# Kernel optimization log

Hardware: AMD Instinct MI355X
Metric: run time of the kernel (lower is better)

## Reference

```python
import jax, jax.numpy as jnp
import numpy as np

B, W, IN, H, Z, D, OUT, K = 256, 128, 128, 1024, 128, 1024, 128, 3


def _gru_cell(h, x, Wih, Whh, bih, bhh):
    # torch nn.GRU single-layer cell, gate order (r, z, n)
    gi = x @ Wih.T + bih
    gh = h @ Whh.T + bhh
    ir, iz, inn = jnp.split(gi, 3, axis=-1)
    hr, hz, hn = jnp.split(gh, 3, axis=-1)
    r = jax.nn.sigmoid(ir + hr)
    u = jax.nn.sigmoid(iz + hz)
    n = jnp.tanh(inn + r * hn)
    return (1.0 - u) * n + u * h


def setup_inputs():
    key = jax.random.key(0)
    ks = iter(jax.random.split(key, 40))

    def w(shape, fanin):
        return jax.random.normal(next(ks), shape, jnp.float32) / np.float32(np.sqrt(fanin))

    return dict(
        x=jax.random.normal(next(ks), (B, W, IN), jnp.float32),
        eps_q=jax.random.uniform(next(ks), (B, W, Z), jnp.float32),
        eps_p=jax.random.uniform(next(ks), (B, W, OUT), jnp.float32),
        Wih_q=w((3 * H, IN), IN), Whh_q=w((3 * H, H), H),
        bih_q=jnp.zeros(3 * H, jnp.float32), bhh_q=jnp.zeros(3 * H, jnp.float32),
        Wd_q=w((D, Z + H), Z + H), bd_q=jnp.zeros(D, jnp.float32),
        Wmu_q=w((Z, D), D), bmu_q=jnp.zeros(Z, jnp.float32),
        Wsig_q=w((Z, D), D), bsig_q=jnp.zeros(Z, jnp.float32),
        Wp=w((K, Z, Z), Z), bp=jnp.zeros((K, Z), jnp.float32),
        up=0.1 * jax.random.normal(next(ks), (K,), jnp.float32),
        Wlg=w((Z, Z), Z), blg=jnp.zeros(Z, jnp.float32),
        Wih_p=w((3 * H, Z), Z), Whh_p=w((3 * H, H), H),
        bih_p=jnp.zeros(3 * H, jnp.float32), bhh_p=jnp.zeros(3 * H, jnp.float32),
        Wd_p=w((D, H), H), bd_p=jnp.zeros(D, jnp.float32),
        Wmu_p=w((OUT, D), D), bmu_p=jnp.zeros(OUT, jnp.float32),
        Wsig_p=w((OUT, D), D), bsig_p=jnp.zeros(OUT, jnp.float32),
    )


def _forward(x, eps_q, eps_p, Wih_q, Whh_q, bih_q, bhh_q, Wd_q, bd_q, Wmu_q, bmu_q,
             Wsig_q, bsig_q, Wp, bp, up, Wlg, blg, Wih_p, Whh_p, bih_p, bhh_p,
             Wd_p, bd_p, Wmu_p, bmu_p, Wsig_p, bsig_p):
    Bsz = x.shape[0]

    # ---- Qnet: sequential encoder with planar flows ----
    def q_step(carry, inp):
        e, z_prev = carry
        x_t, eps_t = inp  # [B,IN], [B,Z]
        e = _gru_cell(e, x_t, Wih_q, Whh_q, bih_q, bhh_q)
        d = jnp.concatenate([z_prev, e], axis=-1) @ Wd_q.T + bd_q
        mu = d @ Wmu_q.T + bmu_q
        logvar = jax.nn.softplus(d @ Wsig_q.T + bsig_q)
        z = mu + jnp.exp(0.5 * logvar) * eps_t
        for k in range(K):  # planar normalizing flows: z + u * tanh(Wz + b)
            z = z + up[k] * jnp.tanh(z @ Wp[k].T + bp[k])
        return (e, z), (z, mu, logvar)

    e0 = jnp.zeros((Bsz, H), x.dtype)
    z0 = jnp.zeros((Bsz, Z), x.dtype)
    _, (z_seq, mu_seq, lv_seq) = jax.lax.scan(
        q_step, (e0, z0), (jnp.swapaxes(x, 0, 1), jnp.swapaxes(eps_q, 0, 1)))

    # ---- Pnet: sequential decoder ----
    def p_step(d_t, inp):
        z_t, eps_t = inp
        zt = z_t @ Wlg.T + blg  # LGSSM linear
        d_t = _gru_cell(d_t, zt, Wih_p, Whh_p, bih_p, bhh_p)
        dd = d_t @ Wd_p.T + bd_p
        mu = dd @ Wmu_p.T + bmu_p
        sigma = jax.nn.softplus(dd @ Wsig_p.T + bsig_p)
        return d_t, mu + sigma * eps_t

    d0 = jnp.zeros((Bsz, H), x.dtype)
    _, out_seq = jax.lax.scan(p_step, d0, (z_seq, jnp.swapaxes(eps_p, 0, 1)))

    return (jnp.swapaxes(out_seq, 0, 1),
            jnp.swapaxes(mu_seq, 0, 1),
            jnp.swapaxes(lv_seq, 0, 1))


def reference(x, eps_q, eps_p, Wih_q, Whh_q, bih_q, bhh_q, Wd_q, bd_q, Wmu_q, bmu_q,
              Wsig_q, bsig_q, Wp, bp, up, Wlg, blg, Wih_p, Whh_p, bih_p, bhh_p,
              Wd_p, bd_p, Wmu_p, bmu_p, Wsig_p, bsig_p):
    return _forward(x, eps_q, eps_p, Wih_q, Whh_q, bih_q, bhh_q, Wd_q, bd_q, Wmu_q,
                    bmu_q, Wsig_q, bsig_q, Wp, bp, up, Wlg, blg, Wih_p, Whh_p,
                    bih_p, bhh_p, Wd_p, bd_p, Wmu_p, bmu_p, Wsig_p, bsig_p)
```

## Files before the change

### kernel.cpp

```cpp
#include <hip/hip_runtime.h>


typedef __bf16 bf16;
typedef __bf16 bf16x4 __attribute__((ext_vector_type(4)));
typedef __bf16 bf16x8 __attribute__((ext_vector_type(8)));
typedef float  f32x4  __attribute__((ext_vector_type(4)));
typedef unsigned long long u64;
typedef unsigned u32;

static constexpr int CB   = 256;
static constexpr int CW   = 128;
static constexpr int CIN  = 128;
static constexpr int CH   = 1024;
static constexpr int CZ   = 128;
static constexpr int CD   = 1024;
static constexpr int COUT = 128;

static constexpr int APITCH     = 1160;
static constexpr int ABUF_BYTES = 16 * APITCH * 2;
static constexpr int REDN       = 8 * 16 * 17;
static constexpr int RED2_BYTES = 2 * REDN * 4;
static constexpr int FLOW_BYTES = (2 * CZ + 2 * 2 * CZ) * 4;
static constexpr int SMEM_BYTES = ABUF_BYTES + RED2_BYTES + FLOW_BYTES;

#define DEV static __device__ __forceinline__

DEV float sigmoidf_(float x) { return 1.0f / (1.0f + expf(-x)); }
DEV float softplusf_(float x) { return x > 20.0f ? x : log1pf(expf(x)); }
DEV bf16x8 ldfrag(const bf16* p) { return *reinterpret_cast<const bf16x8*>(p); }

#define MFMA(a, b, c) __builtin_amdgcn_mfma_f32_16x16x32_bf16((a), (b), (c), 0, 0, 0)

DEV u64 lda8(const void* p) {
    return __hip_atomic_load((const u64*)p, __ATOMIC_RELAXED, __HIP_MEMORY_SCOPE_AGENT);
}
DEV u32 lda4(const void* p) {
    return __hip_atomic_load((const u32*)p, __ATOMIC_RELAXED, __HIP_MEMORY_SCOPE_AGENT);
}
DEV void sta4(void* p, u32 v) {
    __hip_atomic_store((u32*)p, v, __ATOMIC_RELAXED, __HIP_MEMORY_SCOPE_AGENT);
}
DEV bf16x8 ld_act16(const bf16* p) {
    union { u64 u[2]; bf16x8 v; } r;
    r.u[0] = lda8(p);
    r.u[1] = lda8((const char*)p + 8);
    return r.v;
}
DEV u32 pk2(float a, float b) {
    union { bf16 h[2]; u32 u; } r;
    r.h[0] = (bf16)a; r.h[1] = (bf16)b;
    return r.u;
}

struct Prm {
    const float *eps_q, *eps_p;
    const float *bih_q, *bhh_q, *bd_q, *bmu_q, *bsig_q;
    const float *Wp, *bp, *up, *Wlg, *blg;
    const float *bih_p, *bhh_p, *bd_p, *bmu_p, *bsig_p;
    const bf16 *x_b, *Wih_qb, *Whh_qb, *Wd_qb, *Wmu_qb, *Wsg_qb;
    const bf16 *Wih_pb, *Whh_pb, *Wd_pb, *Wmu_pb, *Wsg_pb;
    float *e_f0, *e_f1; bf16 *e_b0, *e_b1;
    float *d_f0, *d_f1; bf16 *d_b0, *d_b1;
    float *ztmp_f;
    bf16 *dvec_b, *ddvec_b;
    bf16 *zflow;
    bf16 *ztlg;
    u32 *barQ, *barP, *zbar;
    float *out_o, *out_mu, *out_lv;
};

DEV void gbar_h(u32* bar, int wgl, u32 k)
{
    asm volatile("s_waitcnt vmcnt(0)" ::: "memory");
    __syncthreads();
    if (threadIdx.x == 0)
        __hip_atomic_store(&bar[wgl], k, __ATOMIC_RELAXED, __HIP_MEMORY_SCOPE_AGENT);
    if (threadIdx.x < 128) {
        while (__hip_atomic_load(&bar[threadIdx.x], __ATOMIC_RELAXED,
                                 __HIP_MEMORY_SCOPE_AGENT) < k)
            __builtin_amdgcn_s_sleep(1);
    }
    __syncthreads();
}

__global__ void k_cvt(const float* __restrict__ src, bf16* __restrict__ dst, int n)
{
    int i = (blockIdx.x * blockDim.x + threadIdx.x) * 4;
    if (i < n) {
        float4 v = *reinterpret_cast<const float4*>(src + i);
        bf16x4 o;
        o[0] = (bf16)v.x; o[1] = (bf16)v.y; o[2] = (bf16)v.z; o[3] = (bf16)v.w;
        *reinterpret_cast<bf16x4*>(dst + i) = o;
    }
}

DEV void stage_act(bf16* abuf, int tid, int r0,
                   const bf16* __restrict__ head, long hs, int K1, int hagent,
                   const bf16* __restrict__ body, long bs)
{
    const int CHN = (K1 + CH) >> 3;
    const int TOT = 16 * CHN;
    for (int idx = tid; idx < TOT; idx += 512) {
        const int row = idx / CHN;
        const int k = (idx - row * CHN) * 8;
        bf16x8 v;
        if (k < K1) {
            const bf16* s = head + (long)(r0 + row) * hs + k;
            v = hagent ? ld_act16(s) : ldfrag(s);
        } else {
            v = ld_act16(body + (long)(r0 + row) * bs + (k - K1));
        }
        *reinterpret_cast<bf16x8*>(abuf + (long)row * APITCH + k) = v;
    }
    __syncthreads();
}

DEV void gru_compute(const Prm& p, const bf16* abuf, int r0, int n0,
                     int lane, int wave,
                     const bf16* __restrict__ Wih, const bf16* __restrict__ Whh,
                     const float* __restrict__ bih, const float* __restrict__ bhh,
                     const float* __restrict__ Efin,
                     float* __restrict__ Efo, bf16* __restrict__ Ebo)
{
    const int lr = lane & 15, lkE = (lane >> 4) * 8;
    const int c = n0 + wave * 16 + lr;
    const bf16* arow = abuf + (long)lr * APITCH;

    f32x4 acc[4] = {};
#pragma unroll 4
    for (int k = 0; k < CIN; k += 32) {
        bf16x8 a = *reinterpret_cast<const bf16x8*>(arow + k + lkE);
#pragma unroll
        for (int g = 0; g < 3; ++g) {
            bf16x8 b = ldfrag(Wih + ((long)g * CH + c) * CIN + k + lkE);
            const int grp = (g == 2) ? 2 : g;
            acc[grp] = MFMA(a, b, acc[grp]);
        }
    }
#pragma unroll 4
    for (int k = 0; k < CH; k += 32) {
        bf16x8 a = *reinterpret_cast<const bf16x8*>(arow + CIN + k + lkE);
#pragma unroll
        for (int g = 0; g < 3; ++g) {
            bf16x8 b = ldfrag(Whh + ((long)g * CH + c) * CH + k + lkE);
            const int grp = (g == 2) ? 3 : g;
            acc[grp] = MFMA(a, b, acc[grp]);
        }
    }

    const float b0r = bih[c] + bhh[c];
    const float b0z = bih[CH + c] + bhh[CH + c];
    const float bin = bih[2 * CH + c];
    const float bhn = bhh[2 * CH + c];
    const int rbase = r0 + (lane >> 4) * 4;
#pragma unroll
    for (int i = 0; i < 4; ++i) {
        const int row = rbase + i;
        float gr = acc[0][i] + b0r;
        float gz = acc[1][i] + b0z;
        float gi = acc[2][i] + bin;
        float gh = acc[3][i] + bhn;
        float r = sigmoidf_(gr);
        float u = sigmoidf_(gz);
        float n = tanhf(gi + r * gh);
        float en = (1.0f - u) * n + u * Efin[(long)row * CH + c];
        Efo[(long)row * CH + c] = en;
        float vB = __shfl_xor(en, 1);
        if (!(lane & 1))
            sta4(Ebo + (long)row * CH + c, pk2(en, vB));
    }
}

DEV void lin_compute(const bf16* abuf, int r0, int n0, int lane, int wave, int Ktot,
                     const bf16* __restrict__ W,
                     const float* __restrict__ bias, bf16* __restrict__ Out)
{
    const int lr = lane & 15, lkE = (lane >> 4) * 8;
    const int c = n0 + wave * 16 + lr;
    const bf16* arow = abuf + (long)lr * APITCH;
    const bf16* wrow = W + (long)c * Ktot;

    f32x4 acc = {};
#pragma unroll 4
    for (int k = 0; k < CH; k += 32) {
        bf16x8 a = *reinterpret_cast<const bf16x8*>(arow + (Ktot - CH) + k + lkE);
        bf16x8 b = ldfrag(wrow + (Ktot - CH) + k + lkE);
        acc = MFMA(a, b, acc);
    }
    if (Ktot > CH) {
#pragma unroll 4
        for (int k = 0; k < CZ; k += 32) {
            bf16x8 a = *reinterpret_cast<const bf16x8*>(arow + k + lkE);
            bf16x8 b = ldfrag(wrow + k + lkE);
            acc = MFMA(a, b, acc);
        }
    }

    const float bb = bias[c];
    const int rbase = r0 + (lane >> 4) * 4;
#pragma unroll
    for (int i = 0; i < 4; ++i) {
        float v = acc[i] + bb;
        float vB = __shfl_xor(v, 1);
        if (!(lane & 1))
            sta4(Out + (long)(rbase + i) * CD + c, pk2(v, vB));
    }
}

template <int MODE>
DEV void phase_tail2(const Prm& p, int t, int wgl, int tid, int lane, int wave,
                     float* Ra, float* Rs, const bf16* __restrict__ A,
                     const bf16* __restrict__ Wa, const bf16* __restrict__ Wb,
                     const float* __restrict__ ba, const float* __restrict__ bb)
{
    const int lr = lane & 15, lkE = (lane >> 4) * 8;
    const int mb = (wgl >> 3) << 4;
    const int nb = (wgl & 7) << 4;
    f32x4 am = {}, as = {};
    const int k0 = wave * 128;
#pragma unroll
    for (int kk = 0; kk < 128; kk += 32) {
        const int k = k0 + kk;
        bf16x8 a  = ld_act16(A + (long)(mb + lr) * CD + k + lkE);
        bf16x8 bm = ldfrag(Wa + (long)(nb + lr) * CD + k + lkE);
        bf16x8 bs = ldfrag(Wb + (long)(nb + lr) * CD + k + lkE);
        am = MFMA(a, bm, am);
        as = MFMA(a, bs, as);
    }
    __syncthreads();
#pragma unroll
    for (int i = 0; i < 4; ++i) {
        Ra[(wave * 16 + (lane >> 4) * 4 + i) * 17 + lr] = am[i];
        Rs[(wave * 16 + (lane >> 4) * 4 + i) * 17 + lr] = as[i];
    }
    __syncthreads();
    if (tid < 256) {
        const int trow = tid >> 4, tcol = tid & 15;
        float vm = 0.f, vs = 0.f;
#pragma unroll
        for (int w = 0; w < 8; ++w) {
            vm += Ra[(w * 16 + trow) * 17 + tcol];
            vs += Rs[(w * 16 + trow) * 17 + tcol];
        }
        const int row = mb + trow, col = nb + tcol;
        if constexpr (MODE == 0) {
            float mu = vm + ba[col];
            float lv = softplusf_(vs + bb[col]);
            float e  = p.eps_q[(long)row * CW * CZ + (long)t * CZ + col];
            float z  = mu + expf(0.5f * lv) * e;
            p.out_mu[(long)row * CW * CZ + (long)t * CZ + col] = mu;
            p.out_lv[(long)row * CW * CZ + (long)t * CZ + col] = lv;
            sta4(p.ztmp_f + (long)row * CZ + col, __float_as_uint(z));
        } else {
            float m  = vm + ba[col];
            float sg = softplusf_(vs + bb[col]);
            float e  = p.eps_p[(long)row * CW * COUT + (long)t * COUT + col];
            p.out_o[(long)row * CW * COUT + (long)t * COUT + col] = m + sg * e;
        }
    }
}

DEV void phase_flows2(const Prm& p, int wgl, int tid, int t, float* zl, float* ps)
{
    const int rg = tid >> 8;
    const int sub = tid & 255;
    const int c = sub & 127, half = sub >> 7;
    const int row = wgl * 2 + rg;
    float* zrow = zl + rg * CZ;
    float* pall = ps + rg * 2 * CZ;

    if (half == 0)
        zrow[c] = __uint_as_float(lda4(p.ztmp_f + (long)row * CZ + c));
    __syncthreads();

#pragma unroll 1
    for (int kf = 0; kf < 3; ++kf) {
        const float* wr = p.Wp + ((long)kf * CZ + c) * CZ + half * 64;
        const float* zh = zrow + half * 64;
        float s = 0.f;
#pragma unroll
        for (int j = 0; j < 64; j += 4) {
            float4 w = *reinterpret_cast<const float4*>(wr + j);
            s += zh[j] * w.x + zh[j + 1] * w.y + zh[j + 2] * w.z + zh[j + 3] * w.w;
        }
        pall[half * CZ + c] = s;
        __syncthreads();
        if (half == 0) {
            float sf = pall[c] + pall[CZ + c] + p.bp[kf * CZ + c];
            zrow[c] += p.up[kf] * tanhf(sf);
        }
        __syncthreads();
    }
    {
        const float* wr = p.Wlg + (long)c * CZ + half * 64;
        const float* zh = zrow + half * 64;
        float s = 0.f;
#pragma unroll
        for (int j = 0; j < 64; j += 4) {
            float4 w = *reinterpret_cast<const float4*>(wr + j);
            s += zh[j] * w.x + zh[j + 1] * w.y + zh[j + 2] * w.z + zh[j + 3] * w.w;
        }
        pall[half * CZ + c] = s;
        __syncthreads();
        if (half == 0) {
            float zt = pall[c] + pall[CZ + c] + p.blg[c];
            float ztB = __shfl_xor(zt, 1);
            if (!(c & 1)) {
                sta4(p.ztlg  + ((size_t)t * CB + row) * CZ + c, pk2(zt, ztB));
                sta4(p.zflow + ((size_t)(t + 1) * CB + row) * CZ + c,
                     pk2(zrow[c], zrow[c + 1]));
            }
        }
    }
}

__launch_bounds__(512)
__global__ void mega(Prm p)
{
    extern __shared__ char smem[];
    bf16*  abuf = (bf16*)smem;
    float* Ra   = (float*)(smem + ABUF_BYTES);
    float* Rs   = Ra + REDN;
    float* ZLp  = (float*)(smem + ABUF_BYTES + RED2_BYTES);
    float* PSp  = ZLp + 2 * CZ;

    const int wg = blockIdx.x, tid = threadIdx.x;
    const int lane = tid & 63, wave = tid >> 6;
    const bool isQ = wg < 128;
    const int wgl = isQ ? wg : wg - 128;
    const int r0 = (wgl >> 3) * 16;
    const int n0 = (wgl & 7) * 128;

    if (isQ) {
        u32 bk = 0;
#pragma unroll 1
        for (int t = 0; t < CW; ++t) {
            const int bi = t & 1;
            const bf16*  eb_i = bi ? p.e_b1 : p.e_b0;
            const float* ef_i = bi ? p.e_f1 : p.e_f0;
            bf16*  eb_o = bi ? p.e_b0 : p.e_b1;
            float* ef_o = bi ? p.e_f0 : p.e_f1;

            stage_act(abuf, tid, r0, p.x_b + (long)t * CIN, (long)CW * CIN, CIN, 0,
                      eb_i, CH);
            gru_compute(p, abuf, r0, n0, lane, wave, p.Wih_qb, p.Whh_qb,
                        p.bih_q, p.bhh_q, ef_i, ef_o, eb_o);
            gbar_h(p.barQ, wgl, ++bk);
            stage_act(abuf, tid, r0, p.zflow + (size_t)t * CB * CZ, CZ, CZ, 1,
                      eb_o, CH);
            lin_compute(abuf, r0, n0, lane, wave, CZ + CH, p.Wd_qb, p.bd_q, p.dvec_b);
            gbar_h(p.barQ, wgl, ++bk);
            phase_tail2<0>(p, t, wgl, tid, lane, wave, Ra, Rs,
                           p.dvec_b, p.Wmu_qb, p.Wsg_qb, p.bmu_q, p.bsig_q);
            gbar_h(p.barQ, wgl, ++bk);
            phase_flows2(p, wgl, tid, t, ZLp, PSp);
            asm volatile("s_waitcnt vmcnt(0)" ::: "memory");
            __syncthreads();
            if (tid == 0)
                __hip_atomic_store(&p.zbar[wgl], (u32)(t + 1),
                                   __ATOMIC_RELAXED, __HIP_MEMORY_SCOPE_AGENT);
            __syncthreads();
        }
    } else {
        u32 bk = 0;
#pragma unroll 1
        for (int t = 0; t < CW; ++t) {
            if (tid < 128) {
                while (__hip_atomic_load(&p.zbar[tid], __ATOMIC_RELAXED,
                                         __HIP_MEMORY_SCOPE_AGENT) < (u32)(t + 1))
                    __builtin_amdgcn_s_sleep(2);
            }
            __syncthreads();

            const int bi = t & 1;
            const bf16*  db_i = bi ? p.d_b1 : p.d_b0;
            const float* df_i = bi ? p.d_f1 : p.d_f0;
            bf16*  db_o = bi ? p.d_b0 : p.d_b1;
            float* df_o = bi ? p.d_f0 : p.d_f1;

            stage_act(abuf, tid, r0, p.ztlg + (size_t)t * CB * CZ, CZ, CZ, 1,
                      db_i, CH);
            gru_compute(p, abuf, r0, n0, lane, wave, p.Wih_pb, p.Whh_pb,
                        p.bih_p, p.bhh_p, df_i, df_o, db_o);
            gbar_h(p.barP, wgl, ++bk);
            stage_act(abuf, tid, r0, nullptr, 0, 0, 0, db_o, CH);
            lin_compute(abuf, r0, n0, lane, wave, CH, p.Wd_pb, p.bd_p, p.ddvec_b);
            gbar_h(p.barP, wgl, ++bk);
            phase_tail2<1>(p, t, wgl, tid, lane, wave, Ra, Rs,
                           p.ddvec_b, p.Wmu_pb, p.Wsg_pb, p.bmu_p, p.bsig_p);
        }
    }
}

extern "C" void kernel_launch(void* const* d_in, const int* in_sizes, int n_in,
                              void* d_out, int out_size, void* d_ws, size_t ws_size,
                              hipStream_t stream)
{
    Prm p;
    const float* x      = (const float*)d_in[0];
    p.eps_q  = (const float*)d_in[1];
    p.eps_p  = (const float*)d_in[2];
    const float* Wih_q  = (const float*)d_in[3];
    const float* Whh_q  = (const float*)d_in[4];
    p.bih_q  = (const float*)d_in[5];
    p.bhh_q  = (const float*)d_in[6];
    const float* Wd_q   = (const float*)d_in[7];
    p.bd_q   = (const float*)d_in[8];
    const float* Wmu_q  = (const float*)d_in[9];
    p.bmu_q  = (const float*)d_in[10];
    const float* Wsig_q = (const float*)d_in[11];
    p.bsig_q = (const float*)d_in[12];
    p.Wp     = (const float*)d_in[13];
    p.bp     = (const float*)d_in[14];
    p.up     = (const float*)d_in[15];
    p.Wlg    = (const float*)d_in[16];
    p.blg    = (const float*)d_in[17];
    const float* Wih_p  = (const float*)d_in[18];
    const float* Whh_p  = (const float*)d_in[19];
    p.bih_p  = (const float*)d_in[20];
    p.bhh_p  = (const float*)d_in[21];
    const float* Wd_p   = (const float*)d_in[22];
    p.bd_p   = (const float*)d_in[23];
    const float* Wmu_p  = (const float*)d_in[24];
    p.bmu_p  = (const float*)d_in[25];
    const float* Wsig_p = (const float*)d_in[26];
    p.bsig_p = (const float*)d_in[27];

    p.out_o  = (float*)d_out;
    p.out_mu = p.out_o + (size_t)CB * CW * COUT;
    p.out_lv = p.out_mu + (size_t)CB * CW * CZ;

    char* wp_ = (char*)d_ws;
    auto carve = [&](size_t bytes) -> void* {
        void* q = (void*)wp_;
        wp_ += (bytes + 255) & ~(size_t)255;
        return q;
    };
    p.e_f0 = (float*)carve((size_t)CB * CH * 4);
    p.e_f1 = (float*)carve((size_t)CB * CH * 4);
    p.e_b0 = (bf16*)carve((size_t)CB * CH * 2);
    p.e_b1 = (bf16*)carve((size_t)CB * CH * 2);
    p.d_f0 = (float*)carve((size_t)CB * CH * 4);
    p.d_f1 = (float*)carve((size_t)CB * CH * 4);
    p.d_b0 = (bf16*)carve((size_t)CB * CH * 2);
    p.d_b1 = (bf16*)carve((size_t)CB * CH * 2);
    p.ztmp_f  = (float*)carve((size_t)CB * CZ * 4);
    p.dvec_b  = (bf16*)carve((size_t)CB * CD * 2);
    p.ddvec_b = (bf16*)carve((size_t)CB * CD * 2);
    p.zflow   = (bf16*)carve((size_t)(CW + 1) * CB * CZ * 2);
    p.ztlg    = (bf16*)carve((size_t)CW * CB * CZ * 2);
    p.barQ    = (u32*)carve(512);
    p.barP    = (u32*)carve(512);
    p.zbar    = (u32*)carve(512);
    bf16* x_b    = (bf16*)carve((size_t)CB * CW * CIN * 2);
    bf16* Wih_qb = (bf16*)carve((size_t)3 * CH * CIN * 2);
    bf16* Whh_qb = (bf16*)carve((size_t)3 * CH * CH * 2);
    bf16* Wd_qb  = (bf16*)carve((size_t)CD * (CZ + CH) * 2);
    bf16* Wmu_qb = (bf16*)carve((size_t)CZ * CD * 2);
    bf16* Wsg_qb = (bf16*)carve((size_t)CZ * CD * 2);
    bf16* Wih_pb = (bf16*)carve((size_t)3 * CH * CZ * 2);
    bf16* Whh_pb = (bf16*)carve((size_t)3 * CH * CH * 2);
    bf16* Wd_pb  = (bf16*)carve((size_t)CD * CH * 2);
    bf16* Wmu_pb = (bf16*)carve((size_t)COUT * CD * 2);
    bf16* Wsg_pb = (bf16*)carve((size_t)COUT * CD * 2);
    p.x_b = x_b;       p.Wih_qb = Wih_qb; p.Whh_qb = Whh_qb;
    p.Wd_qb = Wd_qb;   p.Wmu_qb = Wmu_qb; p.Wsg_qb = Wsg_qb;
    p.Wih_pb = Wih_pb; p.Whh_pb = Whh_pb; p.Wd_pb = Wd_pb;
    p.Wmu_pb = Wmu_pb; p.Wsg_pb = Wsg_pb;

    hipMemsetAsync(p.e_f0, 0, (size_t)CB * CH * 4, stream);
    hipMemsetAsync(p.e_b0, 0, (size_t)CB * CH * 2, stream);
    hipMemsetAsync(p.d_f0, 0, (size_t)CB * CH * 4, stream);
    hipMemsetAsync(p.d_b0, 0, (size_t)CB * CH * 2, stream);
    hipMemsetAsync(p.zflow, 0, (size_t)CB * CZ * 2, stream);
    hipMemsetAsync(p.barQ, 0, 512, stream);
    hipMemsetAsync(p.barP, 0, 512, stream);
    hipMemsetAsync(p.zbar, 0, 512, stream);

    auto cvt = [&](const float* s, bf16* d, size_t n) {
        k_cvt<<<dim3((unsigned)((n / 4 + 255) / 256)), dim3(256), 0, stream>>>(s, d, (int)n);
    };
    cvt(x,      x_b,    (size_t)CB * CW * CIN);
    cvt(Wih_q,  Wih_qb, (size_t)3 * CH * CIN);
    cvt(Whh_q,  Whh_qb, (size_t)3 * CH * CH);
    cvt(Wd_q,   Wd_qb,  (size_t)CD * (CZ + CH));
    cvt(Wmu_q,  Wmu_qb, (size_t)CZ * CD);
    cvt(Wsig_q, Wsg_qb, (size_t)CZ * CD);
    cvt(Wih_p,  Wih_pb, (size_t)3 * CH * CZ);
    cvt(Whh_p,  Whh_pb, (size_t)3 * CH * CH);
    cvt(Wd_p,   Wd_pb,  (size_t)CD * CH);
    cvt(Wmu_p,  Wmu_pb, (size_t)COUT * CD);
    cvt(Wsig_p, Wsg_pb, (size_t)COUT * CD);

    mega<<<dim3(256), dim3(512), SMEM_BYTES, stream>>>(p);
}
```

Baseline: 9.720 ms.

## Split persistent kernel into GRU and aux roles with per-slab flag dataflow

Replaces the grid-wide barriers of the persistent megakernel with fine-grained per-slab flags. Dedicated workgroups now run the GRU recurrences while separate auxiliary workgroups handle the dense, head and flow stages, so those stages can run as a lagged pipeline alongside the recurrence. Hidden-state history is multi-buffered (up to a full sequence when the workspace is large) so producers can run ahead without overwrite hazards. The grid shrinks to 192 workgroups with wider per-wave tiles. This adds complexity in flag offsets and buffer indexing, plus a risk of deadlock or races if the lags are wrong.

```diff
diff --git a/kernel.cpp b/kernel.cpp
--- a/kernel.cpp
+++ b/kernel.cpp
@@ -2,7 +2,6 @@
 
 
 typedef __bf16 bf16;
-typedef __bf16 bf16x4 __attribute__((ext_vector_type(4)));
 typedef __bf16 bf16x8 __attribute__((ext_vector_type(8)));
 typedef float  f32x4  __attribute__((ext_vector_type(4)));
 typedef unsigned long long u64;
@@ -15,13 +14,18 @@
 static constexpr int CZ   = 128;
 static constexpr int CD   = 1024;
 static constexpr int COUT = 128;
-
-static constexpr int APITCH     = 1160;
-static constexpr int ABUF_BYTES = 16 * APITCH * 2;
-static constexpr int REDN       = 8 * 16 * 17;
-static constexpr int RED2_BYTES = 2 * REDN * 4;
-static constexpr int FLOW_BYTES = (2 * CZ + 2 * 2 * CZ) * 4;
-static constexpr int SMEM_BYTES = ABUF_BYTES + RED2_BYTES + FLOW_BYTES;
+static constexpr int APITCH = 1160;
+
+static constexpr int FS   = 16;
+static constexpr int FQG  = 0;
+static constexpr int FQAa = 64;
+static constexpr int FQAb = 80;
+static constexpr int FQAd = 96;
+static constexpr int FPG  = 128;
+static constexpr int FPAa = 192;
+static constexpr int FPAb = 208;
+static constexpr int FPAd = 224;
+static constexpr int NFLAG = 256;
 
 #define DEV static __device__ __forceinline__
 
@@ -50,6 +54,10 @@
     union { bf16 h[2]; u32 u; } r;
     r.h[0] = (bf16)a; r.h[1] = (bf16)b;
     return r.u;
+}
+DEV void poll_ge(const u32* f, int tgt) {
+    if (tgt <= 0) return;
+    while ((int)lda4(f) < tgt) __builtin_amdgcn_s_sleep(2);
 }
 
 struct Prm {
@@ -59,44 +67,35 @@
     const float *bih_p, *bhh_p, *bd_p, *bmu_p, *bsig_p;
     const bf16 *x_b, *Wih_qb, *Whh_qb, *Wd_qb, *Wmu_qb, *Wsg_qb;
     const bf16 *Wih_pb, *Whh_pb, *Wd_pb, *Wmu_pb, *Wsg_pb;
-    float *e_f0, *e_f1; bf16 *e_b0, *e_b1;
-    float *d_f0, *d_f1; bf16 *d_b0, *d_b1;
-    float *ztmp_f;
-    bf16 *dvec_b, *ddvec_b;
-    bf16 *zflow;
+    float *ef, *df;
+    bf16 *e_h, *d_h;
+    bf16 *dvpp, *ddvpp;
     bf16 *ztlg;
-    u32 *barQ, *barP, *zbar;
+    bf16 *zfl;
+    float *shq, *shp;
+    u32 *F;
     float *out_o, *out_mu, *out_lv;
+    int DEm;
+    int big;
 };
-
-DEV void gbar_h(u32* bar, int wgl, u32 k)
-{
-    asm volatile("s_waitcnt vmcnt(0)" ::: "memory");
-    __syncthreads();
-    if (threadIdx.x == 0)
-        __hip_atomic_store(&bar[wgl], k, __ATOMIC_RELAXED, __HIP_MEMORY_SCOPE_AGENT);
-    if (threadIdx.x < 128) {
-        while (__hip_atomic_load(&bar[threadIdx.x], __ATOMIC_RELAXED,
-                                 __HIP_MEMORY_SCOPE_AGENT) < k)
-            __builtin_amdgcn_s_sleep(1);
-    }
-    __syncthreads();
-}
 
 __global__ void k_cvt(const float* __restrict__ src, bf16* __restrict__ dst, int n)
 {
     int i = (blockIdx.x * blockDim.x + threadIdx.x) * 4;
     if (i < n) {
         float4 v = *reinterpret_cast<const float4*>(src + i);
-        bf16x4 o;
-        o[0] = (bf16)v.x; o[1] = (bf16)v.y; o[2] = (bf16)v.z; o[3] = (bf16)v.w;
-        *reinterpret_cast<bf16x4*>(dst + i) = o;
-    }
-}
-
-DEV void stage_act(bf16* abuf, int tid, int r0,
-                   const bf16* __restrict__ head, long hs, int K1, int hagent,
-                   const bf16* __restrict__ body, long bs)
+        bf16 o0 = (bf16)v.x, o1 = (bf16)v.y, o2 = (bf16)v.z, o3 = (bf16)v.w;
+        u32 lo, hi;
+        { union { bf16 h[2]; u32 u; } t; t.h[0]=o0; t.h[1]=o1; lo=t.u; }
+        { union { bf16 h[2]; u32 u; } t; t.h[0]=o2; t.h[1]=o3; hi=t.u; }
+        *reinterpret_cast<u32*>(dst + i) = lo;
+        *reinterpret_cast<u32*>(dst + i + 2) = hi;
+    }
+}
+
+DEV void stage(bf16* abuf, int tid, int r0,
+               const bf16* head, long hrs, int K1, bool hc,
+               const bf16* body, long brs, bool bc)
 {
     const int CHN = (K1 + CH) >> 3;
     const int TOT = 16 * CHN;
@@ -105,211 +104,300 @@
         const int k = (idx - row * CHN) * 8;
         bf16x8 v;
         if (k < K1) {
-            const bf16* s = head + (long)(r0 + row) * hs + k;
-            v = hagent ? ld_act16(s) : ldfrag(s);
+            const bf16* s = head + (long)(r0 + row) * hrs + k;
+            v = hc ? ldfrag(s) : ld_act16(s);
         } else {
-            v = ld_act16(body + (long)(r0 + row) * bs + (k - K1));
+            const bf16* s = body + (long)(r0 + row) * brs + (k - K1);
+            v = bc ? ldfrag(s) : ld_act16(s);
         }
         *reinterpret_cast<bf16x8*>(abuf + (long)row * APITCH + k) = v;
     }
     __syncthreads();
 }
 
-DEV void gru_compute(const Prm& p, const bf16* abuf, int r0, int n0,
-                     int lane, int wave,
-                     const bf16* __restrict__ Wih, const bf16* __restrict__ Whh,
-                     const float* __restrict__ bih, const float* __restrict__ bhh,
-                     const float* __restrict__ Efin,
-                     float* __restrict__ Efo, bf16* __restrict__ Ebo)
+DEV void gru2(const bf16* abuf, int r0, int colbase, int lane,
+              const bf16* __restrict__ Wih, const bf16* __restrict__ Whh,
+              const float* __restrict__ bih, const float* __restrict__ bhh,
+              const float* __restrict__ efin, float* __restrict__ efout,
+              bf16* __restrict__ ehout)
 {
     const int lr = lane & 15, lkE = (lane >> 4) * 8;
-    const int c = n0 + wave * 16 + lr;
     const bf16* arow = abuf + (long)lr * APITCH;
-
-    f32x4 acc[4] = {};
+    f32x4 acc[2][4] = {};
+
 #pragma unroll 4
     for (int k = 0; k < CIN; k += 32) {
         bf16x8 a = *reinterpret_cast<const bf16x8*>(arow + k + lkE);
 #pragma unroll
-        for (int g = 0; g < 3; ++g) {
-            bf16x8 b = ldfrag(Wih + ((long)g * CH + c) * CIN + k + lkE);
-            const int grp = (g == 2) ? 2 : g;
-            acc[grp] = MFMA(a, b, acc[grp]);
+        for (int j = 0; j < 2; ++j) {
+            const int c = colbase + j * 16 + lr;
+#pragma unroll
+            for (int g = 0; g < 3; ++g) {
+                bf16x8 b = ldfrag(Wih + ((long)g * CH + c) * CIN + k + lkE);
+                const int grp = (g == 2) ? 2 : g;
+                acc[j][grp] = MFMA(a, b, acc[j][grp]);
+            }
         }
     }
 #pragma unroll 4
     for (int k = 0; k < CH; k += 32) {
         bf16x8 a = *reinterpret_cast<const bf16x8*>(arow + CIN + k + lkE);
 #pragma unroll
-        for (int g = 0; g < 3; ++g) {
-            bf16x8 b = ldfrag(Whh + ((long)g * CH + c) * CH + k + lkE);
-            const int grp = (g == 2) ? 3 : g;
-            acc[grp] = MFMA(a, b, acc[grp]);
-        }
-    }
-
-    const float b0r = bih[c] + bhh[c];
-    const float b0z = bih[CH + c] + bhh[CH + c];
-    const float bin = bih[2 * CH + c];
-    const float bhn = bhh[2 * CH + c];
-    const int rbase = r0 + (lane >> 4) * 4;
-#pragma unroll
-    for (int i = 0; i < 4; ++i) {
-        const int row = rbase + i;
-        float gr = acc[0][i] + b0r;
-        float gz = acc[1][i] + b0z;
-        float gi = acc[2][i] + bin;
-        float gh = acc[3][i] + bhn;
-        float r = sigmoidf_(gr);
-        float u = sigmoidf_(gz);
-        float n = tanhf(gi + r * gh);
-        float en = (1.0f - u) * n + u * Efin[(long)row * CH + c];
-        Efo[(long)row * CH + c] = en;
-        float vB = __shfl_xor(en, 1);
-        if (!(lane & 1))
-            sta4(Ebo + (long)row * CH + c, pk2(en, vB));
-    }
-}
-
-DEV void lin_compute(const bf16* abuf, int r0, int n0, int lane, int wave, int Ktot,
-                     const bf16* __restrict__ W,
-                     const float* __restrict__ bias, bf16* __restrict__ Out)
+        for (int j = 0; j < 2; ++j) {
+            const int c = colbase + j * 16 + lr;
+#pragma unroll
+            for (int g = 0; g < 3; ++g) {
+                bf16x8 b = ldfrag(Whh + ((long)g * CH + c) * CH + k + lkE);
+                const int grp = (g == 2) ? 3 : g;
+                acc[j][grp] = MFMA(a, b, acc[j][grp]);
+            }
+        }
+    }
+#pragma unroll
+    for (int j = 0; j < 2; ++j) {
+        const int c = colbase + j * 16 + lr;
+        const float b0r = bih[c] + bhh[c];
+        const float b0z = bih[CH + c] + bhh[CH + c];
+        const float bin = bih[2 * CH + c];
+        const float bhn = bhh[2 * CH + c];
+#pragma unroll
+        for (int i = 0; i < 4; ++i) {
+            const int row = r0 + (lane >> 4) * 4 + i;
+            float r = sigmoidf_(acc[j][0][i] + b0r);
+            float u = sigmoidf_(acc[j][1][i] + b0z);
+            float n = tanhf(acc[j][2][i] + bin + r * (acc[j][3][i] + bhn));
+            float en = (1.0f - u) * n + u * efin[(long)row * CH + c];
+            efout[(long)row * CH + c] = en;
+            float vB = __shfl_xor(en, 1);
+            if (!(lane & 1))
+                sta4(ehout + (long)row * CH + c, pk2(en, vB));
+        }
+    }
+}
+
+DEV void lin4(const bf16* abuf, int r0, int c0, int lane, int Ktot,
+              const bf16* __restrict__ W, const float* __restrict__ bias,
+              bf16* __restrict__ outb)
 {
     const int lr = lane & 15, lkE = (lane >> 4) * 8;
-    const int c = n0 + wave * 16 + lr;
     const bf16* arow = abuf + (long)lr * APITCH;
-    const bf16* wrow = W + (long)c * Ktot;
-
+    f32x4 acc[4] = {};
+#pragma unroll 4
+    for (int k = 0; k < Ktot; k += 32) {
+        bf16x8 a = *reinterpret_cast<const bf16x8*>(arow + k + lkE);
+#pragma unroll
+        for (int j = 0; j < 4; ++j) {
+            const int c = c0 + j * 16 + lr;
+            bf16x8 b = ldfrag(W + (long)c * Ktot + k + lkE);
+            acc[j] = MFMA(a, b, acc[j]);
+        }
+    }
+#pragma unroll
+    for (int j = 0; j < 4; ++j) {
+        const int c = c0 + j * 16 + lr;
+        const float bb = bias[c];
+#pragma unroll
+        for (int i = 0; i < 4; ++i) {
+            const int row = r0 + (lane >> 4) * 4 + i;
+            float v = acc[j][i] + bb;
+            float vB = __shfl_xor(v, 1);
+            if (!(lane & 1))
+                sta4(outb + (long)row * CD + c, pk2(v, vB));
+        }
+    }
+}
+
+DEV f32x4 head16(const bf16* abuf, int lane, int c2, const bf16* __restrict__ W)
+{
+    const int lr = lane & 15, lkE = (lane >> 4) * 8;
+    const bf16* arow = abuf + (long)lr * APITCH;
+    const bf16* wrow = W + (long)c2 * CD;
     f32x4 acc = {};
 #pragma unroll 4
-    for (int k = 0; k < CH; k += 32) {
-        bf16x8 a = *reinterpret_cast<const bf16x8*>(arow + (Ktot - CH) + k + lkE);
-        bf16x8 b = ldfrag(wrow + (Ktot - CH) + k + lkE);
+    for (int k = 0; k < CD; k += 32) {
+        bf16x8 a = *reinterpret_cast<const bf16x8*>(arow + k + lkE);
+        bf16x8 b = ldfrag(wrow + k + lkE);
         acc = MFMA(a, b, acc);
     }
-    if (Ktot > CH) {
-#pragma unroll 4
-        for (int k = 0; k < CZ; k += 32) {
-            bf16x8 a = *reinterpret_cast<const bf16x8*>(arow + k + lkE);
-            bf16x8 b = ldfrag(wrow + k + lkE);
-            acc = MFMA(a, b, acc);
-        }
-    }
-
-    const float bb = bias[c];
-    const int rbase = r0 + (lane >> 4) * 4;
-#pragma unroll
-    for (int i = 0; i < 4; ++i) {
-        float v = acc[i] + bb;
-        float vB = __shfl_xor(v, 1);
-        if (!(lane & 1))
-            sta4(Out + (long)(rbase + i) * CD + c, pk2(v, vB));
-    }
-}
-
-template <int MODE>
-DEV void phase_tail2(const Prm& p, int t, int wgl, int tid, int lane, int wave,
-                     float* Ra, float* Rs, const bf16* __restrict__ A,
-                     const bf16* __restrict__ Wa, const bf16* __restrict__ Wb,
-                     const float* __restrict__ ba, const float* __restrict__ bb)
-{
-    const int lr = lane & 15, lkE = (lane >> 4) * 8;
-    const int mb = (wgl >> 3) << 4;
-    const int nb = (wgl & 7) << 4;
-    f32x4 am = {}, as = {};
-    const int k0 = wave * 128;
-#pragma unroll
-    for (int kk = 0; kk < 128; kk += 32) {
-        const int k = k0 + kk;
-        bf16x8 a  = ld_act16(A + (long)(mb + lr) * CD + k + lkE);
-        bf16x8 bm = ldfrag(Wa + (long)(nb + lr) * CD + k + lkE);
-        bf16x8 bs = ldfrag(Wb + (long)(nb + lr) * CD + k + lkE);
-        am = MFMA(a, bm, am);
-        as = MFMA(a, bs, as);
-    }
-    __syncthreads();
-#pragma unroll
-    for (int i = 0; i < 4; ++i) {
-        Ra[(wave * 16 + (lane >> 4) * 4 + i) * 17 + lr] = am[i];
-        Rs[(wave * 16 + (lane >> 4) * 4 + i) * 17 + lr] = as[i];
-    }
-    __syncthreads();
-    if (tid < 256) {
-        const int trow = tid >> 4, tcol = tid & 15;
-        float vm = 0.f, vs = 0.f;
-#pragma unroll
-        for (int w = 0; w < 8; ++w) {
-            vm += Ra[(w * 16 + trow) * 17 + tcol];
-            vs += Rs[(w * 16 + trow) * 17 + tcol];
-        }
-        const int row = mb + trow, col = nb + tcol;
-        if constexpr (MODE == 0) {
-            float mu = vm + ba[col];
-            float lv = softplusf_(vs + bb[col]);
-            float e  = p.eps_q[(long)row * CW * CZ + (long)t * CZ + col];
-            float z  = mu + expf(0.5f * lv) * e;
-            p.out_mu[(long)row * CW * CZ + (long)t * CZ + col] = mu;
-            p.out_lv[(long)row * CW * CZ + (long)t * CZ + col] = lv;
-            sta4(p.ztmp_f + (long)row * CZ + col, __float_as_uint(z));
+    return acc;
+}
+
+DEV void do_flows(const Prm& p, float* zbuf, int tid, int t, int slab)
+{
+    const int r = tid >> 5;
+    const int c0 = (tid & 31) * 4;
+    for (int kf = 0; kf < 3; ++kf) {
+        float s0 = p.bp[kf * CZ + c0],     s1 = p.bp[kf * CZ + c0 + 1];
+        float s2 = p.bp[kf * CZ + c0 + 2], s3 = p.bp[kf * CZ + c0 + 3];
+        const float* w0 = p.Wp + ((long)kf * CZ + c0) * CZ;
+#pragma unroll 8
+        for (int j = 0; j < CZ; j += 4) {
+            float4 z4 = *reinterpret_cast<const float4*>(&zbuf[r * CZ + j]);
+            float4 a0 = *reinterpret_cast<const float4*>(w0 + j);
+            float4 a1 = *reinterpret_cast<const float4*>(w0 + CZ + j);
+            float4 a2 = *reinterpret_cast<const float4*>(w0 + 2 * CZ + j);
+            float4 a3 = *reinterpret_cast<const float4*>(w0 + 3 * CZ + j);
+            s0 += z4.x * a0.x + z4.y * a0.y + z4.z * a0.z + z4.w * a0.w;
+            s1 += z4.x * a1.x + z4.y * a1.y + z4.z * a1.z + z4.w * a1.w;
+            s2 += z4.x * a2.x + z4.y * a2.y + z4.z * a2.z + z4.w * a2.w;
+            s3 += z4.x * a3.x + z4.y * a3.y + z4.z * a3.z + z4.w * a3.w;
+        }
+        const float uk = p.up[kf];
+        __syncthreads();
+        zbuf[r * CZ + c0]     += uk * tanhf(s0);
+        zbuf[r * CZ + c0 + 1] += uk * tanhf(s1);
+        zbuf[r * CZ + c0 + 2] += uk * tanhf(s2);
+        zbuf[r * CZ + c0 + 3] += uk * tanhf(s3);
+        __syncthreads();
+    }
+    float s0 = p.blg[c0], s1 = p.blg[c0 + 1], s2 = p.blg[c0 + 2], s3 = p.blg[c0 + 3];
+    const float* w0 = p.Wlg + (long)c0 * CZ;
+#pragma unroll 8
+    for (int j = 0; j < CZ; j += 4) {
+        float4 z4 = *reinterpret_cast<const float4*>(&zbuf[r * CZ + j]);
+        float4 a0 = *reinterpret_cast<const float4*>(w0 + j);
+        float4 a1 = *reinterpret_cast<const float4*>(w0 + CZ + j);
+        float4 a2 = *reinterpret_cast<const float4*>(w0 + 2 * CZ + j);
+        float4 a3 = *reinterpret_cast<const float4*>(w0 + 3 * CZ + j);
+        s0 += z4.x * a0.x + z4.y * a0.y + z4.z * a0.z + z4.w * a0.w;
+        s1 += z4.x * a1.x + z4.y * a1.y + z4.z * a1.z + z4.w * a1.w;
+        s2 += z4.x * a2.x + z4.y * a2.y + z4.z * a2.z + z4.w * a2.w;
+        s3 += z4.x * a3.x + z4.y * a3.y + z4.z * a3.z + z4.w * a3.w;
+    }
+    const int grow = slab * 16 + r;
+    bf16* zt = p.ztlg + ((size_t)t * CB + grow) * CZ + c0;
+    sta4(zt,     pk2(s0, s1));
+    sta4(zt + 2, pk2(s2, s3));
+    bf16* zf = p.zfl + ((size_t)(t & 3) * CB + grow) * CZ + c0;
+    sta4(zf,     pk2(zbuf[r * CZ + c0],     zbuf[r * CZ + c0 + 1]));
+    sta4(zf + 2, pk2(zbuf[r * CZ + c0 + 2], zbuf[r * CZ + c0 + 3]));
+}
+
+DEV void run_gru_role(const Prm& p, bf16* abuf, int slab, int slice,
+                      const bf16* headbase, long hstep, long hrs,
+                      const bf16* Wih, const bf16* Whh,
+                      const float* bih, const float* bhh,
+                      float* efm, bf16* hist, int fSelf,
+                      int w4f, int w4o, int w5f, int w5o, int w6f, int w6o)
+{
+    const int tid = threadIdx.x, lane = tid & 63, wave = tid >> 6;
+    const int r0 = slab * 16;
+    const int colbase = slice * 256 + wave * 32;
+    u32* F = p.F;
+    const int DEm = p.DEm;
+    const bool big = p.big != 0;
+
+    for (int t = 0; t < CW; ++t) {
+        if (tid < 4)       poll_ge(F + (fSelf + slab * 4 + tid) * FS, t);
+        else if (tid == 4) poll_ge(F + w4f * FS, t + w4o);
+        else if (tid == 5 && w5f >= 0) poll_ge(F + w5f * FS, t + w5o);
+        else if (tid == 6 && w6f >= 0) poll_ge(F + w6f * FS, t + w6o);
+        __syncthreads();
+
+        stage(abuf, tid, r0, headbase + (long)t * hstep, hrs, CIN, true,
+              hist + (size_t)((t - 1) & DEm) * CB * CH, CH, big);
+
+        gru2(abuf, r0, colbase, lane, Wih, Whh, bih, bhh,
+             efm + (size_t)(t & 1) * CB * CH,
+             efm + (size_t)((t & 1) ^ 1) * CB * CH,
+             hist + (size_t)(t & DEm) * CB * CH);
+
+        asm volatile("s_waitcnt vmcnt(0)" ::: "memory");
+        __syncthreads();
+        if (tid == 0) sta4(F + (fSelf + slab * 4 + slice) * FS, (u32)(t + 1));
+    }
+}
+
+DEV void run_aux_role(const Prm& p, bf16* abuf, float* zbuf,
+                      int slab, int half, bool isQ)
+{
+    const int tid = threadIdx.x, lane = tid & 63, wave = tid >> 6;
+    const int r0 = slab * 16;
+    const int c2 = wave * 16 + (lane & 15);
+    u32* F = p.F;
+    const int DEm = p.DEm;
+    const bool big = p.big != 0;
+
+    const int fG  = isQ ? FQG : FPG;
+    const int fD  = (isQ ? FQAd : FPAd) + slab * 2;
+    const int fB  = (isQ ? FQAb : FPAb) + slab;
+    const int fA  = (isQ ? FQAa : FPAa) + slab;
+    const bf16* Wlin = isQ ? p.Wd_qb : p.Wd_pb;
+    const int   Klin = isQ ? (CZ + CH) : CH;
+    const float* blin = isQ ? p.bd_q : p.bd_p;
+    bf16* dv = isQ ? p.dvpp : p.ddvpp;
+    float* sh = isQ ? p.shq : p.shp;
+    const bf16* Wmu = isQ ? p.Wmu_qb : p.Wmu_pb;
+    const bf16* Wsg = isQ ? p.Wsg_qb : p.Wsg_pb;
+    const bf16* hist = isQ ? p.e_h : p.d_h;
+
+    for (int t = 0; t < CW; ++t) {
+        if (tid < 4)              poll_ge(F + (fG + slab * 4 + tid) * FS, t + 1);
+        else if (tid == 4 && isQ) poll_ge(F + fA * FS, t);
+        __syncthreads();
+
+        if (isQ)
+            stage(abuf, tid, r0, p.zfl + (size_t)((t - 1) & 3) * CB * CZ, CZ, CZ, false,
+                  hist + (size_t)(t & DEm) * CB * CH, CH, big);
+        else
+            stage(abuf, tid, r0, nullptr, 0, 0, false,
+                  hist + (size_t)(t & DEm) * CB * CH, CH, big);
+
+        lin4(abuf, r0, half * 512 + wave * 64, lane, Klin, Wlin, blin,
+             dv + (size_t)(t & 1) * CB * CD);
+        asm volatile("s_waitcnt vmcnt(0)" ::: "memory");
+        __syncthreads();
+        if (tid == 0) {
+            sta4(F + (fD + half) * FS, (u32)(t + 1));
+            poll_ge(F + (fD + (half ^ 1)) * FS, t + 1);
+        }
+        __syncthreads();
+
+        stage(abuf, tid, r0, nullptr, 0, 0, false,
+              dv + (size_t)(t & 1) * CB * CD, CD, false);
+
+        if (half == 1) {
+            f32x4 vs = head16(abuf, lane, c2, Wsg);
+            float* shw = sh + (size_t)(t & 1) * CB * CZ;
+#pragma unroll
+            for (int i = 0; i < 4; ++i) {
+                const int row = r0 + (lane >> 4) * 4 + i;
+                sta4(shw + (size_t)row * CZ + c2, __float_as_uint(vs[i]));
+            }
+            asm volatile("s_waitcnt vmcnt(0)" ::: "memory");
+            __syncthreads();
+            if (tid == 0) sta4(F + fB * FS, (u32)(t + 1));
         } else {
-            float m  = vm + ba[col];
-            float sg = softplusf_(vs + bb[col]);
-            float e  = p.eps_p[(long)row * CW * COUT + (long)t * COUT + col];
-            p.out_o[(long)row * CW * COUT + (long)t * COUT + col] = m + sg * e;
-        }
-    }
-}
-
-DEV void phase_flows2(const Prm& p, int wgl, int tid, int t, float* zl, float* ps)
-{
-    const int rg = tid >> 8;
-    const int sub = tid & 255;
-    const int c = sub & 127, half = sub >> 7;
-    const int row = wgl * 2 + rg;
-    float* zrow = zl + rg * CZ;
-    float* pall = ps + rg * 2 * CZ;
-
-    if (half == 0)
-        zrow[c] = __uint_as_float(lda4(p.ztmp_f + (long)row * CZ + c));
-    __syncthreads();
-
-#pragma unroll 1
-    for (int kf = 0; kf < 3; ++kf) {
-        const float* wr = p.Wp + ((long)kf * CZ + c) * CZ + half * 64;
-        const float* zh = zrow + half * 64;
-        float s = 0.f;
-#pragma unroll
-        for (int j = 0; j < 64; j += 4) {
-            float4 w = *reinterpret_cast<const float4*>(wr + j);
-            s += zh[j] * w.x + zh[j + 1] * w.y + zh[j + 2] * w.z + zh[j + 3] * w.w;
-        }
-        pall[half * CZ + c] = s;
-        __syncthreads();
-        if (half == 0) {
-            float sf = pall[c] + pall[CZ + c] + p.bp[kf * CZ + c];
-            zrow[c] += p.up[kf] * tanhf(sf);
-        }
-        __syncthreads();
-    }
-    {
-        const float* wr = p.Wlg + (long)c * CZ + half * 64;
-        const float* zh = zrow + half * 64;
-        float s = 0.f;
-#pragma unroll
-        for (int j = 0; j < 64; j += 4) {
-            float4 w = *reinterpret_cast<const float4*>(wr + j);
-            s += zh[j] * w.x + zh[j + 1] * w.y + zh[j + 2] * w.z + zh[j + 3] * w.w;
-        }
-        pall[half * CZ + c] = s;
-        __syncthreads();
-        if (half == 0) {
-            float zt = pall[c] + pall[CZ + c] + p.blg[c];
-            float ztB = __shfl_xor(zt, 1);
-            if (!(c & 1)) {
-                sta4(p.ztlg  + ((size_t)t * CB + row) * CZ + c, pk2(zt, ztB));
-                sta4(p.zflow + ((size_t)(t + 1) * CB + row) * CZ + c,
-                     pk2(zrow[c], zrow[c + 1]));
+            f32x4 vm = head16(abuf, lane, c2, Wmu);
+            if (tid == 0) poll_ge(F + fB * FS, t + 1);
+            __syncthreads();
+            const float* shr = sh + (size_t)(t & 1) * CB * CZ;
+#pragma unroll
+            for (int i = 0; i < 4; ++i) {
+                const int row = r0 + (lane >> 4) * 4 + i;
+                float vs = __uint_as_float(lda4(shr + (size_t)row * CZ + c2));
+                if (isQ) {
+                    float mu = vm[i] + p.bmu_q[c2];
+                    float lv = softplusf_(vs + p.bsig_q[c2]);
+                    float e  = p.eps_q[(size_t)row * CW * CZ + (size_t)t * CZ + c2];
+                    float z  = mu + expf(0.5f * lv) * e;
+                    p.out_mu[(size_t)row * CW * CZ + (size_t)t * CZ + c2] = mu;
+                    p.out_lv[(size_t)row * CW * CZ + (size_t)t * CZ + c2] = lv;
+                    zbuf[((lane >> 4) * 4 + i) * CZ + c2] = z;
+                } else {
+                    float m  = vm[i] + p.bmu_p[c2];
+                    float sg = softplusf_(vs + p.bsig_p[c2]);
+                    float e  = p.eps_p[(size_t)row * CW * COUT + (size_t)t * COUT + c2];
+                    p.out_o[(size_t)row * CW * COUT + (size_t)t * COUT + c2] = m + sg * e;
+                }
             }
+            if (isQ) {
+                __syncthreads();
+                do_flows(p, zbuf, tid, t, slab);
+            }
+            asm volatile("s_waitcnt vmcnt(0)" ::: "memory");
+            __syncthreads();
+            if (tid == 0) sta4(F + fA * FS, (u32)(t + 1));
         }
     }
 }
@@ -317,78 +405,28 @@
 __launch_bounds__(512)
 __global__ void mega(Prm p)
 {
-    extern __shared__ char smem[];
-    bf16*  abuf = (bf16*)smem;
-    float* Ra   = (float*)(smem + ABUF_BYTES);
-    float* Rs   = Ra + REDN;
-    float* ZLp  = (float*)(smem + ABUF_BYTES + RED2_BYTES);
-    float* PSp  = ZLp + 2 * CZ;
-
-    const int wg = blockIdx.x, tid = threadIdx.x;
-    const int lane = tid & 63, wave = tid >> 6;
-    const bool isQ = wg < 128;
-    const int wgl = isQ ? wg : wg - 128;
-    const int r0 = (wgl >> 3) * 16;
-    const int n0 = (wgl & 7) * 128;
-
-    if (isQ) {
-        u32 bk = 0;
-#pragma unroll 1
-        for (int t = 0; t < CW; ++t) {
-            const int bi = t & 1;
-            const bf16*  eb_i = bi ? p.e_b1 : p.e_b0;
-            const float* ef_i = bi ? p.e_f1 : p.e_f0;
-            bf16*  eb_o = bi ? p.e_b0 : p.e_b1;
-            float* ef_o = bi ? p.e_f0 : p.e_f1;
-
-            stage_act(abuf, tid, r0, p.x_b + (long)t * CIN, (long)CW * CIN, CIN, 0,
-                      eb_i, CH);
-            gru_compute(p, abuf, r0, n0, lane, wave, p.Wih_qb, p.Whh_qb,
-                        p.bih_q, p.bhh_q, ef_i, ef_o, eb_o);
-            gbar_h(p.barQ, wgl, ++bk);
-            stage_act(abuf, tid, r0, p.zflow + (size_t)t * CB * CZ, CZ, CZ, 1,
-                      eb_o, CH);
-            lin_compute(abuf, r0, n0, lane, wave, CZ + CH, p.Wd_qb, p.bd_q, p.dvec_b);
-            gbar_h(p.barQ, wgl, ++bk);
-            phase_tail2<0>(p, t, wgl, tid, lane, wave, Ra, Rs,
-                           p.dvec_b, p.Wmu_qb, p.Wsg_qb, p.bmu_q, p.bsig_q);
-            gbar_h(p.barQ, wgl, ++bk);
-            phase_flows2(p, wgl, tid, t, ZLp, PSp);
-            asm volatile("s_waitcnt vmcnt(0)" ::: "memory");
-            __syncthreads();
-            if (tid == 0)
-                __hip_atomic_store(&p.zbar[wgl], (u32)(t + 1),
-                                   __ATOMIC_RELAXED, __HIP_MEMORY_SCOPE_AGENT);
-            __syncthreads();
-        }
+    __shared__ bf16  abuf[16 * APITCH];
+    __shared__ float zbuf[16 * CZ];
+    const int wg = blockIdx.x;
+
+    if (wg < 64) {
+        const int slab = wg >> 2, slice = wg & 3;
+        run_gru_role(p, abuf, slab, slice,
+                     p.x_b, (long)CIN, (long)CW * CIN,
+                     p.Wih_qb, p.Whh_qb, p.bih_q, p.bhh_q,
+                     p.ef, p.e_h, FQG,
+                     FQAa + slab, -3, FQAb + slab, -3, -1, 0);
+    } else if (wg < 96) {
+        run_aux_role(p, abuf, zbuf, (wg - 64) >> 1, (wg - 64) & 1, true);
+    } else if (wg < 160) {
+        const int slab = (wg - 96) >> 2, slice = (wg - 96) & 3;
+        run_gru_role(p, abuf, slab, slice,
+                     p.ztlg, (long)CB * CZ, (long)CZ,
+                     p.Wih_pb, p.Whh_pb, p.bih_p, p.bhh_p,
+                     p.df, p.d_h, FPG,
+                     FQAa + slab, +1, FPAa + slab, -3, FPAb + slab, -3);
     } else {
-        u32 bk = 0;
-#pragma unroll 1
-        for (int t = 0; t < CW; ++t) {
-            if (tid < 128) {
-                while (__hip_atomic_load(&p.zbar[tid], __ATOMIC_RELAXED,
-                                         __HIP_MEMORY_SCOPE_AGENT) < (u32)(t + 1))
-                    __builtin_amdgcn_s_sleep(2);
-            }
-            __syncthreads();
-
-            const int bi = t & 1;
-            const bf16*  db_i = bi ? p.d_b1 : p.d_b0;
-            const float* df_i = bi ? p.d_f1 : p.d_f0;
-            bf16*  db_o = bi ? p.d_b0 : p.d_b1;
-            float* df_o = bi ? p.d_f0 : p.d_f1;
-
-            stage_act(abuf, tid, r0, p.ztlg + (size_t)t * CB * CZ, CZ, CZ, 1,
-                      db_i, CH);
-            gru_compute(p, abuf, r0, n0, lane, wave, p.Wih_pb, p.Whh_pb,
-                        p.bih_p, p.bhh_p, df_i, df_o, db_o);
-            gbar_h(p.barP, wgl, ++bk);
-            stage_act(abuf, tid, r0, nullptr, 0, 0, 0, db_o, CH);
-            lin_compute(abuf, r0, n0, lane, wave, CH, p.Wd_pb, p.bd_p, p.ddvec_b);
-            gbar_h(p.barP, wgl, ++bk);
-            phase_tail2<1>(p, t, wgl, tid, lane, wave, Ra, Rs,
-                           p.ddvec_b, p.Wmu_pb, p.Wsg_pb, p.bmu_p, p.bsig_p);
-        }
+        run_aux_role(p, abuf, zbuf, (wg - 160) >> 1, (wg - 160) & 1, false);
     }
 }
 
@@ -430,28 +468,27 @@
     p.out_mu = p.out_o + (size_t)CB * CW * COUT;
     p.out_lv = p.out_mu + (size_t)CB * CW * CZ;
 
+    const int DE = (ws_size >= (size_t)200 * 1024 * 1024) ? 128 : 4;
+    p.DEm = DE - 1;
+    p.big = (DE == 128) ? 1 : 0;
+
     char* wp_ = (char*)d_ws;
     auto carve = [&](size_t bytes) -> void* {
         void* q = (void*)wp_;
         wp_ += (bytes + 255) & ~(size_t)255;
         return q;
     };
-    p.e_f0 = (float*)carve((size_t)CB * CH * 4);
-    p.e_f1 = (float*)carve((size_t)CB * CH * 4);
-    p.e_b0 = (bf16*)carve((size_t)CB * CH * 2);
-    p.e_b1 = (bf16*)carve((size_t)CB * CH * 2);
-    p.d_f0 = (float*)carve((size_t)CB * CH * 4);
-    p.d_f1 = (float*)carve((size_t)CB * CH * 4);
-    p.d_b0 = (bf16*)carve((size_t)CB * CH * 2);
-    p.d_b1 = (bf16*)carve((size_t)CB * CH * 2);
-    p.ztmp_f  = (float*)carve((size_t)CB * CZ * 4);
-    p.dvec_b  = (bf16*)carve((size_t)CB * CD * 2);
-    p.ddvec_b = (bf16*)carve((size_t)CB * CD * 2);
-    p.zflow   = (bf16*)carve((size_t)(CW + 1) * CB * CZ * 2);
-    p.ztlg    = (bf16*)carve((size_t)CW * CB * CZ * 2);
-    p.barQ    = (u32*)carve(512);
-    p.barP    = (u32*)carve(512);
-    p.zbar    = (u32*)carve(512);
+    p.ef    = (float*)carve((size_t)2 * CB * CH * 4);
+    p.df    = (float*)carve((size_t)2 * CB * CH * 4);
+    p.e_h   = (bf16*)carve((size_t)DE * CB * CH * 2);
+    p.d_h   = (bf16*)carve((size_t)DE * CB * CH * 2);
+    p.dvpp  = (bf16*)carve((size_t)2 * CB * CD * 2);
+    p.ddvpp = (bf16*)carve((size_t)2 * CB * CD * 2);
+    p.ztlg  = (bf16*)carve((size_t)CW * CB * CZ * 2);
+    p.zfl   = (bf16*)carve((size_t)4 * CB * CZ * 2);
+    p.shq   = (float*)carve((size_t)2 * CB * CZ * 4);
+    p.shp   = (float*)carve((size_t)2 * CB * CZ * 4);
+    p.F     = (u32*)carve((size_t)NFLAG * FS * 4);
     bf16* x_b    = (bf16*)carve((size_t)CB * CW * CIN * 2);
     bf16* Wih_qb = (bf16*)carve((size_t)3 * CH * CIN * 2);
     bf16* Whh_qb = (bf16*)carve((size_t)3 * CH * CH * 2);
@@ -468,14 +505,12 @@
     p.Wih_pb = Wih_pb; p.Whh_pb = Whh_pb; p.Wd_pb = Wd_pb;
     p.Wmu_pb = Wmu_pb; p.Wsg_pb = Wsg_pb;
 
-    hipMemsetAsync(p.e_f0, 0, (size_t)CB * CH * 4, stream);
-    hipMemsetAsync(p.e_b0, 0, (size_t)CB * CH * 2, stream);
-    hipMemsetAsync(p.d_f0, 0, (size_t)CB * CH * 4, stream);
-    hipMemsetAsync(p.d_b0, 0, (size_t)CB * CH * 2, stream);
-    hipMemsetAsync(p.zflow, 0, (size_t)CB * CZ * 2, stream);
-    hipMemsetAsync(p.barQ, 0, 512, stream);
-    hipMemsetAsync(p.barP, 0, 512, stream);
-    hipMemsetAsync(p.zbar, 0, 512, stream);
+    hipMemsetAsync(p.ef, 0, (size_t)CB * CH * 4, stream);
+    hipMemsetAsync(p.df, 0, (size_t)CB * CH * 4, stream);
+    hipMemsetAsync(p.e_h + (size_t)(DE - 1) * CB * CH, 0, (size_t)CB * CH * 2, stream);
+    hipMemsetAsync(p.d_h + (size_t)(DE - 1) * CB * CH, 0, (size_t)CB * CH * 2, stream);
+    hipMemsetAsync(p.zfl, 0, (size_t)4 * CB * CZ * 2, stream);
+    hipMemsetAsync(p.F, 0, (size_t)NFLAG * FS * 4, stream);
 
     auto cvt = [&](const float* s, bf16* d, size_t n) {
         k_cvt<<<dim3((unsigned)((n / 4 + 255) / 256)), dim3(256), 0, stream>>>(s, d, (int)n);
@@ -492,5 +527,5 @@
     cvt(Wmu_p,  Wmu_pb, (size_t)COUT * CD);
     cvt(Wsig_p, Wsg_pb, (size_t)COUT * CD);
 
-    mega<<<dim3(256), dim3(512), SMEM_BYTES, stream>>>(p);
-}
+    mega<<<dim3(192), dim3(512), 0, stream>>>(p);
+}
```

After: 21.18 ms. 2.18x slower.
